# Optimization experiments

Measured on AMD Instinct MI355X. Metric: run time of the kernel, lower is better.

Reference implementation:

```python
import jax, jax.numpy as jnp
import numpy as np

D_MODEL = 1024
N_HEADS = 16
D_K = D_MODEL // N_HEADS
ROPE_THETA = 10000.0


def setup_inputs() -> dict:
    key = jax.random.key(0)
    ks = jax.random.split(key, 5)
    B, S = 2, 2048
    std = (2.0 / (D_MODEL + D_MODEL)) ** 0.5
    x = jax.random.normal(ks[0], (B, S, D_MODEL), dtype=jnp.float32)
    Wq = jax.random.normal(ks[1], (D_MODEL, D_MODEL), dtype=jnp.float32) * std
    Wk = jax.random.normal(ks[2], (D_MODEL, D_MODEL), dtype=jnp.float32) * std
    Wv = jax.random.normal(ks[3], (D_MODEL, D_MODEL), dtype=jnp.float32) * std
    Wo = jax.random.normal(ks[4], (D_MODEL, D_MODEL), dtype=jnp.float32) * std
    token_positions = jnp.arange(S, dtype=jnp.int64 if jax.config.jax_enable_x64 else jnp.int32)
    return {"x": x, "Wq": Wq, "Wk": Wk, "Wv": Wv, "Wo": Wo,
            "token_positions": token_positions}


def _apply_rope(t, token_positions):
    # t: [B, H, S, d_k]; token_positions: [S]
    inv_freq = 1.0 / (ROPE_THETA ** (jnp.arange(0, D_K, 2, dtype=jnp.float32) / D_K))  # [d_k/2]
    freqs = token_positions.astype(jnp.float32)[:, None] * inv_freq[None, :]  # [S, d_k/2]
    cos, sin = jnp.cos(freqs), jnp.sin(freqs)
    x1, x2 = t[..., ::2], t[..., 1::2]
    xr = x1 * cos - x2 * sin
    yr = x1 * sin + x2 * cos
    # interleave back to even/odd positions
    out = jnp.stack([xr, yr], axis=-1).reshape(t.shape)
    return out


def reference(x, Wq, Wk, Wv, Wo, token_positions):
    B, S, D = x.shape
    H, dk = N_HEADS, D_K
    # projections: weight is [d_out, d_in], applied as x @ W.T
    def proj_heads(W):
        y = jnp.einsum('bsd,ed->bse', x, W)
        return y.reshape(B, S, H, dk).transpose(0, 2, 1, 3)  # [B,H,S,dk]
    q = proj_heads(Wq)
    k = proj_heads(Wk)
    v = proj_heads(Wv)
    q = _apply_rope(q, token_positions)
    k = _apply_rope(k, token_positions)
    scores = jnp.einsum('bhqd,bhkd->bhqk', q, k) / jnp.sqrt(jnp.float32(dk))
    causal = jnp.tril(jnp.ones((S, S), dtype=bool))
    scores = jnp.where(causal, scores, -jnp.inf)
    attn = jax.nn.softmax(scores, axis=-1)
    out = jnp.einsum('bhqk,bhkd->bhqd', attn, v)  # [B,H,S,dk]
    out = out.transpose(0, 2, 1, 3).reshape(B, S, D)
    return jnp.einsum('bsd,ed->bse', out, Wo)
```

## Files before the change

### kernel.cpp

```cpp
#include <hip/hip_runtime.h>

typedef __bf16 bf16x8 __attribute__((ext_vector_type(8)));
typedef float f32x4 __attribute__((ext_vector_type(4)));
typedef unsigned short u16x8 __attribute__((ext_vector_type(8)));


__device__ __forceinline__ unsigned short f2bf(float f) {
  unsigned u = __builtin_bit_cast(unsigned, f);
  u = (u + 0x7FFFu + ((u >> 16) & 1u)) >> 16;
  return (unsigned short)u;
}

__device__ __forceinline__ void load_lds16(const void* g, void* l) {
  __builtin_amdgcn_global_load_lds(
      (__attribute__((address_space(1))) void*)g,
      (__attribute__((address_space(3))) void*)l, 16, 0, 0);
}

__global__ __launch_bounds__(256) void k_convert(
    const float* __restrict__ x,
    const float* __restrict__ wq, const float* __restrict__ wk,
    const float* __restrict__ wv, const float* __restrict__ wo,
    unsigned short* __restrict__ xb,
    unsigned short* __restrict__ wqb, unsigned short* __restrict__ wkb,
    unsigned short* __restrict__ wvb, unsigned short* __restrict__ wob) {
  const int g = blockIdx.x * 256 + threadIdx.x;
  const float* src;
  unsigned short* dst;
  int off;
  if (g < (1 << 20)) {
    src = x; dst = xb; off = g;
  } else {
    const int q = g - (1 << 20);
    const int t = q >> 18;
    off = q & ((1 << 18) - 1);
    src = (t == 0) ? wq : (t == 1) ? wk : (t == 2) ? wv : wo;
    dst = (t == 0) ? wqb : (t == 1) ? wkb : (t == 2) ? wvb : wob;
  }
  const float4 v = ((const float4*)src)[off];
  ushort4 r;
  r.x = f2bf(v.x); r.y = f2bf(v.y); r.z = f2bf(v.z); r.w = f2bf(v.w);
  ((ushort4*)dst)[off] = r;
}

__global__ __launch_bounds__(256) void k_rope_tab(const int* __restrict__ tpos,
                                                  float* __restrict__ ct,
                                                  float* __restrict__ st) {
  const int idx = blockIdx.x * 256 + threadIdx.x;
  const int s = idx >> 5, i = idx & 31;
  const double p = (double)tpos[s];
  const double f = p * pow(10000.0, -(double)(2 * i) / 64.0);
  ct[idx] = (float)cos(f);
  st[idx] = (float)sin(f);
}

__device__ __forceinline__ void gemm_core_1024(
    const unsigned short* __restrict__ Ag,
    const unsigned short* __restrict__ Bg,
    unsigned short* As, unsigned short* Bs, f32x4 (&acc)[4][4], int tid) {
  const int lane = tid & 63;
  const int w = tid >> 6;
  const int wm = (w >> 1) * 64;
  const int wn = (w & 1) * 64;
  const int lr = lane & 15;
  const int lg8 = (lane >> 4) * 8;
  const int c0 = tid, c1 = 256 + tid;
  const int ar0 = c0 >> 2, ac0 = (c0 & 3) * 8;
  const int ar1 = c1 >> 2, ac1 = (c1 & 3) * 8;

  auto stage = [&](int buf, int kt) {
    unsigned short* Ab = As + buf * 4096;
    unsigned short* Bb = Bs + buf * 4096;
    load_lds16(Ag + ar0 * 1024 + kt + ac0, Ab + c0 * 8);
    load_lds16(Ag + ar1 * 1024 + kt + ac1, Ab + c1 * 8);
    load_lds16(Bg + ar0 * 1024 + kt + ac0, Bb + c0 * 8);
    load_lds16(Bg + ar1 * 1024 + kt + ac1, Bb + c1 * 8);
  };

  stage(0, 0);
  stage(1, 32);
  int cur = 0;
  for (int ki = 0; ki < 32; ++ki) {
    if (ki + 2 < 32) {
      int nb = cur + 2; if (nb >= 3) nb -= 3;
      stage(nb, (ki + 2) * 32);
      asm volatile("s_waitcnt vmcnt(8)" ::: "memory");
    } else if (ki + 1 < 32) {
      asm volatile("s_waitcnt vmcnt(4)" ::: "memory");
    } else {
      asm volatile("s_waitcnt vmcnt(0)" ::: "memory");
    }
    __builtin_amdgcn_s_barrier();
    const unsigned short* Ab = As + cur * 4096;
    const unsigned short* Bb = Bs + cur * 4096;
    bf16x8 af[4], bfv[4];
#pragma unroll
    for (int mi = 0; mi < 4; ++mi)
      af[mi] = *(const bf16x8*)(Ab + (wm + mi * 16 + lr) * 32 + lg8);
#pragma unroll
    for (int ni = 0; ni < 4; ++ni)
      bfv[ni] = *(const bf16x8*)(Bb + (wn + ni * 16 + lr) * 32 + lg8);
    __builtin_amdgcn_s_setprio(1);
#pragma unroll
    for (int mi = 0; mi < 4; ++mi)
#pragma unroll
      for (int ni = 0; ni < 4; ++ni)
        acc[mi][ni] = __builtin_amdgcn_mfma_f32_16x16x32_bf16(
            af[mi], bfv[ni], acc[mi][ni], 0, 0, 0);
    __builtin_amdgcn_s_setprio(0);
    __builtin_amdgcn_s_barrier();
    ++cur; if (cur == 3) cur = 0;
  }
}

__global__ __launch_bounds__(256) void k_proj(
    const unsigned short* __restrict__ Xb,
    const unsigned short* __restrict__ Wq, const unsigned short* __restrict__ Wk,
    const unsigned short* __restrict__ Wv,
    const float* __restrict__ ctab, const float* __restrict__ stab,
    unsigned short* __restrict__ Qo, unsigned short* __restrict__ Ko,
    unsigned short* __restrict__ Vo) {
  __shared__ __align__(16) unsigned short As[3 * 128 * 32];
  __shared__ __align__(16) unsigned short Bs[3 * 128 * 32];
  const int z = blockIdx.z;
  const unsigned short* Wsel = (z == 0) ? Wq : (z == 1) ? Wk : Wv;
  unsigned short* Out = (z == 0) ? Qo : (z == 1) ? Ko : Vo;
  const int tid = threadIdx.x;
  const int bm = blockIdx.x * 128, bn = blockIdx.y * 128;
  f32x4 acc[4][4] = {};
  gemm_core_1024(Xb + (size_t)bm * 1024, Wsel + (size_t)bn * 1024, As, Bs, acc, tid);

  const int lane = tid & 63, w = tid >> 6;
  const int wm = (w >> 1) * 64, wn = (w & 1) * 64;
  const int lr = lane & 15, lg = lane >> 4;
  const bool rope = (z < 2);
  const bool odd = lane & 1;
#pragma unroll
  for (int mi = 0; mi < 4; ++mi) {
#pragma unroll
    for (int ni = 0; ni < 4; ++ni) {
#pragma unroll
      for (int reg = 0; reg < 4; ++reg) {
        const int r = bm + wm + mi * 16 + lg * 4 + reg;
        const int e = bn + wn + ni * 16 + lr;
        float val = acc[mi][ni][reg];
        const float partner = __shfl_xor(val, 1);
        const int s = r & 2047, b = r >> 11;
        const int h = e >> 6, d = e & 63;
        float outv = val;
        if (rope) {
          const int i = d >> 1;
          const float c = ctab[s * 32 + i];
          const float sn = stab[s * 32 + i];
          outv = odd ? (val * c + partner * sn) : (val * c - partner * sn);
        }
        if (z == 2)
          Out[((size_t)(b * 16 + h) * 64 + d) * 2048 + s] = f2bf(outv);
        else
          Out[((size_t)(b * 16 + h) * 2048 + s) * 64 + d] = f2bf(outv);
      }
    }
  }
}

__global__ __launch_bounds__(64, 2) void k_attn(
    const unsigned short* __restrict__ Q, const unsigned short* __restrict__ K,
    const unsigned short* __restrict__ Vt, unsigned short* __restrict__ O) {
  __shared__ __align__(16) unsigned short Vs[64 * 64];
  __shared__ __align__(16) unsigned short Pl[32 * 68];
  const int L = blockIdx.x;
  const int bh = (L & 7) * 4 + ((L >> 3) & 3);
  const int p = L >> 5;
  const int qrowA = p * 16, qrowB = (127 - p) * 16;
  const int lane = threadIdx.x & 63;
  const int lr = lane & 15, lg = lane >> 4;
  const unsigned short* Qg = Q + (size_t)bh * 2048 * 64;
  const unsigned short* Kg = K + (size_t)bh * 2048 * 64;
  const unsigned short* Vg = Vt + (size_t)bh * 64 * 2048;
  const int Ta = (qrowA + 79) >> 6;
  const int Tb = (qrowB + 79) >> 6;

  bf16x8 qfA[2], qfB[2];
#pragma unroll
  for (int h = 0; h < 2; ++h) {
    qfA[h] = *(const bf16x8*)(Qg + (qrowA + lr) * 64 + h * 32 + lg * 8);
    qfB[h] = *(const bf16x8*)(Qg + (qrowB + lr) * 64 + h * 32 + lg * 8);
  }

  u16x8 ouv;
#pragma unroll
  for (int j = 0; j < 8; ++j) ouv[j] = 0x3F80;
  const bf16x8 onesf = __builtin_bit_cast(bf16x8, ouv);

  f32x4 oA[4] = {}, oB[4] = {};
  float mA[4], lA[4], mB[4], lB[4];
#pragma unroll
  for (int r = 0; r < 4; ++r) {
    mA[r] = -__builtin_inff(); lA[r] = 0.f;
    mB[r] = -__builtin_inff(); lB[r] = 0.f;
  }

  const float SCL = 0.125f * 1.44269504088896f;

  const int kbase = lr * 64 + lg * 8;
  const unsigned short* Knext = Kg;
  const int vbase = (lane >> 3) * 2048 + (((lane & 7) ^ (lane >> 3)) * 8);
  const unsigned short* Vnext = Vg;
  unsigned short* Vw = &Vs[0];

  auto loadK = [&](bf16x8 (&kd)[4][2]) {
#pragma unroll
    for (int nt = 0; nt < 4; ++nt)
#pragma unroll
      for (int h = 0; h < 2; ++h)
        kd[nt][h] = *(const bf16x8*)(Knext + nt * 1024 + h * 32 + kbase);
    Knext += 4096;
  };
  auto issueV = [&]() {
#pragma unroll
    for (int i0 = 0; i0 < 8; ++i0)
      load_lds16(Vnext + i0 * 16384 + vbase, Vw + i0 * 512 + lane * 8);
    Vnext += 64;
  };

  auto softmax = [&](f32x4 (&s)[4], float (&m)[4], float (&l)[4], f32x4 (&oa)[4],
                     int qrow, bool needmask, int kv0, int rowbase) {
    float pm[4];
#pragma unroll
    for (int r = 0; r < 4; ++r) pm[r] = -__builtin_inff();
#pragma unroll
    for (int nt = 0; nt < 4; ++nt)
#pragma unroll
      for (int reg = 0; reg < 4; ++reg) {
        float sv = s[nt][reg];
        if (needmask) {
          const int kg = kv0 + nt * 16 + lr;
          const int qg = qrow + lg * 4 + reg;
          if (kg > qg) sv = -__builtin_inff();
        }
        s[nt][reg] = sv;
        pm[reg] = fmaxf(pm[reg], sv);
      }
#pragma unroll
    for (int off = 1; off < 16; off <<= 1)
#pragma unroll
      for (int reg = 0; reg < 4; ++reg)
        pm[reg] = fmaxf(pm[reg], __shfl_xor(pm[reg], off));

    float gm = -1.f;
#pragma unroll
    for (int reg = 0; reg < 4; ++reg) gm = fmaxf(gm, pm[reg] - m[reg]);
    float msc[4];
    if (__any(gm > 0.f)) {
#pragma unroll
      for (int reg = 0; reg < 4; ++reg) {
        const float mn = fmaxf(m[reg], pm[reg]);
        const float al = exp2f(SCL * (m[reg] - mn));
        m[reg] = mn;
        msc[reg] = SCL * mn;
        l[reg] *= al;
#pragma unroll
        for (int nt = 0; nt < 4; ++nt) oa[nt][reg] *= al;
      }
    } else {
#pragma unroll
      for (int reg = 0; reg < 4; ++reg) msc[reg] = SCL * m[reg];
    }
#pragma unroll
    for (int nt = 0; nt < 4; ++nt)
#pragma unroll
      for (int reg = 0; reg < 4; ++reg) {
        const float pv = exp2f(s[nt][reg] * SCL - msc[reg]);
        Pl[(rowbase + lg * 4 + reg) * 68 + nt * 16 + lr] = f2bf(pv);
      }
  };

  bf16x8 kA_[4][2], kB_[4][2];
  loadK(kA_);
  issueV();

  auto body = [&](int t, bf16x8 (&kc)[4][2], bf16x8 (&kn)[4][2]) {
    const int kv0 = t * 64;
    const bool more = (t + 1 < Tb);
    const bool actA = (t < Ta);
    if (more) loadK(kn);

    f32x4 sB_[4];
    __builtin_amdgcn_s_setprio(1);
#pragma unroll
    for (int nt = 0; nt < 4; ++nt) {
      f32x4 z = {0.f, 0.f, 0.f, 0.f};
      z = __builtin_amdgcn_mfma_f32_16x16x32_bf16(qfB[0], kc[nt][0], z, 0, 0, 0);
      sB_[nt] = __builtin_amdgcn_mfma_f32_16x16x32_bf16(qfB[1], kc[nt][1], z, 0, 0, 0);
    }
    __builtin_amdgcn_s_setprio(0);
    softmax(sB_, mB, lB, oB, qrowB, t == Tb - 1, kv0, 16);

    if (actA) {
      f32x4 sA_[4];
      __builtin_amdgcn_s_setprio(1);
#pragma unroll
      for (int nt = 0; nt < 4; ++nt) {
        f32x4 z = {0.f, 0.f, 0.f, 0.f};
        z = __builtin_amdgcn_mfma_f32_16x16x32_bf16(qfA[0], kc[nt][0], z, 0, 0, 0);
        sA_[nt] = __builtin_amdgcn_mfma_f32_16x16x32_bf16(qfA[1], kc[nt][1], z, 0, 0, 0);
      }
      __builtin_amdgcn_s_setprio(0);
      softmax(sA_, mA, lA, oA, qrowA, t == Ta - 1, kv0, 0);
    }

    bf16x8 paA[2], paB[2];
#pragma unroll
    for (int ks = 0; ks < 2; ++ks) {
      paB[ks] = *(const bf16x8*)(Pl + (16 + lr) * 68 + ks * 32 + lg * 8);
      if (actA) paA[ks] = *(const bf16x8*)(Pl + lr * 68 + ks * 32 + lg * 8);
    }

    if (more) asm volatile("s_waitcnt vmcnt(8)" ::: "memory");
    else      asm volatile("s_waitcnt vmcnt(0)" ::: "memory");

    __builtin_amdgcn_s_setprio(1);
    {
      f32x4 z = {0.f, 0.f, 0.f, 0.f};
      z = __builtin_amdgcn_mfma_f32_16x16x32_bf16(paB[0], onesf, z, 0, 0, 0);
      z = __builtin_amdgcn_mfma_f32_16x16x32_bf16(paB[1], onesf, z, 0, 0, 0);
#pragma unroll
      for (int reg = 0; reg < 4; ++reg) lB[reg] += z[reg];
    }
    if (actA) {
      f32x4 z = {0.f, 0.f, 0.f, 0.f};
      z = __builtin_amdgcn_mfma_f32_16x16x32_bf16(paA[0], onesf, z, 0, 0, 0);
      z = __builtin_amdgcn_mfma_f32_16x16x32_bf16(paA[1], onesf, z, 0, 0, 0);
#pragma unroll
      for (int reg = 0; reg < 4; ++reg) lA[reg] += z[reg];
    }
#pragma unroll
    for (int nt = 0; nt < 4; ++nt) {
      const int row = nt * 16 + lr;
      const bf16x8 vb0 = *(const bf16x8*)(Vw + row * 64 + ((lg ^ (row & 7)) * 8));
      const bf16x8 vb1 = *(const bf16x8*)(Vw + row * 64 + (((lg + 4) ^ (row & 7)) * 8));
      oB[nt] = __builtin_amdgcn_mfma_f32_16x16x32_bf16(paB[0], vb0, oB[nt], 0, 0, 0);
      oB[nt] = __builtin_amdgcn_mfma_f32_16x16x32_bf16(paB[1], vb1, oB[nt], 0, 0, 0);
      if (actA) {
        oA[nt] = __builtin_amdgcn_mfma_f32_16x16x32_bf16(paA[0], vb0, oA[nt], 0, 0, 0);
        oA[nt] = __builtin_amdgcn_mfma_f32_16x16x32_bf16(paA[1], vb1, oA[nt], 0, 0, 0);
      }
    }
    __builtin_amdgcn_s_setprio(0);

    asm volatile("s_waitcnt lgkmcnt(0)" ::: "memory");
    if (more) issueV();
  };

  int t = 0;
  for (;;) {
    body(t, kA_, kB_); ++t; if (t >= Tb) break;
    body(t, kB_, kA_); ++t; if (t >= Tb) break;
  }

  const int b = bh >> 4, h = bh & 15;
#pragma unroll
  for (int reg = 0; reg < 4; ++reg) {
    const float invA = 1.0f / lA[reg];
    const float invB = 1.0f / lB[reg];
    const int sA_ = qrowA + lg * 4 + reg;
    const int sB_ = qrowB + lg * 4 + reg;
#pragma unroll
    for (int nt = 0; nt < 4; ++nt) {
      const int dv = nt * 16 + lr;
      O[((size_t)b * 2048 + sA_) * 1024 + h * 64 + dv] = f2bf(oA[nt][reg] * invA);
      O[((size_t)b * 2048 + sB_) * 1024 + h * 64 + dv] = f2bf(oB[nt][reg] * invB);
    }
  }
}

__global__ __launch_bounds__(256) void k_out(const unsigned short* __restrict__ Ab,
                                             const unsigned short* __restrict__ Wo,
                                             float* __restrict__ Out) {
  __shared__ __align__(16) unsigned short As[3 * 128 * 32];
  __shared__ __align__(16) unsigned short Bs[3 * 128 * 32];
  const int tid = threadIdx.x;
  const int bm = blockIdx.x * 128, bn = blockIdx.y * 128;
  f32x4 acc[4][4] = {};
  gemm_core_1024(Ab + (size_t)bm * 1024, Wo + (size_t)bn * 1024, As, Bs, acc, tid);
  const int lane = tid & 63, w = tid >> 6;
  const int wm = (w >> 1) * 64, wn = (w & 1) * 64;
  const int lr = lane & 15, lg = lane >> 4;
#pragma unroll
  for (int mi = 0; mi < 4; ++mi)
#pragma unroll
    for (int ni = 0; ni < 4; ++ni)
#pragma unroll
      for (int reg = 0; reg < 4; ++reg) {
        const int r = bm + wm + mi * 16 + lg * 4 + reg;
        const int e = bn + wn + ni * 16 + lr;
        Out[(size_t)r * 1024 + e] = acc[mi][ni][reg];
      }
}

extern "C" void kernel_launch(void* const* d_in, const int* in_sizes, int n_in,
                              void* d_out, int out_size, void* d_ws, size_t ws_size,
                              hipStream_t stream) {
  const float* x = (const float*)d_in[0];
  const float* Wq = (const float*)d_in[1];
  const float* Wk = (const float*)d_in[2];
  const float* Wv = (const float*)d_in[3];
  const float* Wo = (const float*)d_in[4];
  const int* tpos = (const int*)d_in[5];
  float* out = (float*)d_out;
  char* ws = (char*)d_ws;
  const size_t MB = 1024 * 1024;
  unsigned short* xb = (unsigned short*)(ws);
  unsigned short* wqb = (unsigned short*)(ws + 8 * MB);
  unsigned short* wkb = (unsigned short*)(ws + 10 * MB);
  unsigned short* wvb = (unsigned short*)(ws + 12 * MB);
  unsigned short* wob = (unsigned short*)(ws + 14 * MB);
  unsigned short* Qb = (unsigned short*)(ws + 16 * MB);
  unsigned short* Kb = (unsigned short*)(ws + 24 * MB);
  unsigned short* Vtb = (unsigned short*)(ws + 32 * MB);
  unsigned short* Ab = (unsigned short*)(ws + 40 * MB);
  float* ctab = (float*)(ws + 48 * MB);
  float* stab = (float*)(ws + 48 * MB + 256 * 1024);

  k_convert<<<dim3(8192), dim3(256), 0, stream>>>(x, Wq, Wk, Wv, Wo, xb, wqb, wkb,
                                                  wvb, wob);
  k_rope_tab<<<dim3(256), dim3(256), 0, stream>>>(tpos, ctab, stab);
  k_proj<<<dim3(32, 8, 3), dim3(256), 0, stream>>>(xb, wqb, wkb, wvb, ctab, stab,
                                                   Qb, Kb, Vtb);
  k_attn<<<dim3(2048), dim3(64), 0, stream>>>(Qb, Kb, Vtb, Ab);
  k_out<<<dim3(32, 8), dim3(256), 0, stream>>>(Ab, wob, out);
}
```

Measured before the change: 158.6 us.

## Split paired causal q-tiles into independent single-tile attention blocks

Each attention block previously processed two 16-row query tiles (p and 127-p) so every block did the same amount of causal work. Now each block handles one 16-row tile, the grid is doubled to 4096, and launch bounds allow 4 waves per SIMD. The K register double-buffering is dropped, so K loads are issued inside each iteration and waited on before use. P is converted with the packed v_cvt_pk_bf16_f32 instruction. Per-block work becomes uneven (early tiles are tiny), so load balance now depends on the scheduler, and the exposed K load latency may hurt unless the added occupancy hides it.

```diff
diff --git a/kernel.cpp b/kernel.cpp
--- a/kernel.cpp
+++ b/kernel.cpp
@@ -9,6 +9,12 @@
   unsigned u = __builtin_bit_cast(unsigned, f);
   u = (u + 0x7FFFu + ((u >> 16) & 1u)) >> 16;
   return (unsigned short)u;
+}
+
+__device__ __forceinline__ unsigned cvt_pk_bf16(float lo, float hi) {
+  unsigned r;
+  asm("v_cvt_pk_bf16_f32 %0, %1, %2" : "=v"(r) : "v"(lo), "v"(hi));
+  return r;
 }
 
 __device__ __forceinline__ void load_lds16(const void* g, void* l) {
@@ -163,42 +169,36 @@
   }
 }
 
-__global__ __launch_bounds__(64, 2) void k_attn(
+__global__ __launch_bounds__(64, 4) void k_attn(
     const unsigned short* __restrict__ Q, const unsigned short* __restrict__ K,
     const unsigned short* __restrict__ Vt, unsigned short* __restrict__ O) {
   __shared__ __align__(16) unsigned short Vs[64 * 64];
-  __shared__ __align__(16) unsigned short Pl[32 * 68];
+  __shared__ __align__(16) unsigned short Pl[16 * 68];
   const int L = blockIdx.x;
   const int bh = (L & 7) * 4 + ((L >> 3) & 3);
   const int p = L >> 5;
-  const int qrowA = p * 16, qrowB = (127 - p) * 16;
+  const int qrow = p * 16;
+  const int T = (qrow + 79) >> 6;
   const int lane = threadIdx.x & 63;
   const int lr = lane & 15, lg = lane >> 4;
   const unsigned short* Qg = Q + (size_t)bh * 2048 * 64;
   const unsigned short* Kg = K + (size_t)bh * 2048 * 64;
   const unsigned short* Vg = Vt + (size_t)bh * 64 * 2048;
-  const int Ta = (qrowA + 79) >> 6;
-  const int Tb = (qrowB + 79) >> 6;
-
-  bf16x8 qfA[2], qfB[2];
-#pragma unroll
-  for (int h = 0; h < 2; ++h) {
-    qfA[h] = *(const bf16x8*)(Qg + (qrowA + lr) * 64 + h * 32 + lg * 8);
-    qfB[h] = *(const bf16x8*)(Qg + (qrowB + lr) * 64 + h * 32 + lg * 8);
-  }
+
+  bf16x8 qf[2];
+#pragma unroll
+  for (int h = 0; h < 2; ++h)
+    qf[h] = *(const bf16x8*)(Qg + (qrow + lr) * 64 + h * 32 + lg * 8);
 
   u16x8 ouv;
 #pragma unroll
   for (int j = 0; j < 8; ++j) ouv[j] = 0x3F80;
   const bf16x8 onesf = __builtin_bit_cast(bf16x8, ouv);
 
-  f32x4 oA[4] = {}, oB[4] = {};
-  float mA[4], lA[4], mB[4], lB[4];
-#pragma unroll
-  for (int r = 0; r < 4; ++r) {
-    mA[r] = -__builtin_inff(); lA[r] = 0.f;
-    mB[r] = -__builtin_inff(); lB[r] = 0.f;
-  }
+  f32x4 oacc[4] = {};
+  float m[4], l[4];
+#pragma unroll
+  for (int r = 0; r < 4; ++r) { m[r] = -__builtin_inff(); l[r] = 0.f; }
 
   const float SCL = 0.125f * 1.44269504088896f;
 
@@ -208,14 +208,6 @@
   const unsigned short* Vnext = Vg;
   unsigned short* Vw = &Vs[0];
 
-  auto loadK = [&](bf16x8 (&kd)[4][2]) {
-#pragma unroll
-    for (int nt = 0; nt < 4; ++nt)
-#pragma unroll
-      for (int h = 0; h < 2; ++h)
-        kd[nt][h] = *(const bf16x8*)(Knext + nt * 1024 + h * 32 + kbase);
-    Knext += 4096;
-  };
   auto issueV = [&]() {
 #pragma unroll
     for (int i0 = 0; i0 < 8; ++i0)
@@ -223,8 +215,28 @@
     Vnext += 64;
   };
 
-  auto softmax = [&](f32x4 (&s)[4], float (&m)[4], float (&l)[4], f32x4 (&oa)[4],
-                     int qrow, bool needmask, int kv0, int rowbase) {
+  issueV();
+
+  for (int t = 0; t < T; ++t) {
+    bf16x8 kd[4][2];
+#pragma unroll
+    for (int nt = 0; nt < 4; ++nt)
+#pragma unroll
+      for (int h = 0; h < 2; ++h)
+        kd[nt][h] = *(const bf16x8*)(Knext + nt * 1024 + h * 32 + kbase);
+    Knext += 4096;
+
+    f32x4 sacc[4];
+    __builtin_amdgcn_s_setprio(1);
+#pragma unroll
+    for (int nt = 0; nt < 4; ++nt) {
+      f32x4 z = {0.f, 0.f, 0.f, 0.f};
+      z = __builtin_amdgcn_mfma_f32_16x16x32_bf16(qf[0], kd[nt][0], z, 0, 0, 0);
+      sacc[nt] = __builtin_amdgcn_mfma_f32_16x16x32_bf16(qf[1], kd[nt][1], z, 0, 0, 0);
+    }
+    __builtin_amdgcn_s_setprio(0);
+
+    const bool needmask = (t == T - 1);
     float pm[4];
 #pragma unroll
     for (int r = 0; r < 4; ++r) pm[r] = -__builtin_inff();
@@ -232,13 +244,13 @@
     for (int nt = 0; nt < 4; ++nt)
 #pragma unroll
       for (int reg = 0; reg < 4; ++reg) {
-        float sv = s[nt][reg];
+        float sv = sacc[nt][reg];
         if (needmask) {
-          const int kg = kv0 + nt * 16 + lr;
+          const int kg = t * 64 + nt * 16 + lr;
           const int qg = qrow + lg * 4 + reg;
           if (kg > qg) sv = -__builtin_inff();
         }
-        s[nt][reg] = sv;
+        sacc[nt][reg] = sv;
         pm[reg] = fmaxf(pm[reg], sv);
       }
 #pragma unroll
@@ -260,116 +272,65 @@
         msc[reg] = SCL * mn;
         l[reg] *= al;
 #pragma unroll
-        for (int nt = 0; nt < 4; ++nt) oa[nt][reg] *= al;
+        for (int nt = 0; nt < 4; ++nt) oacc[nt][reg] *= al;
       }
     } else {
 #pragma unroll
       for (int reg = 0; reg < 4; ++reg) msc[reg] = SCL * m[reg];
     }
-#pragma unroll
-    for (int nt = 0; nt < 4; ++nt)
-#pragma unroll
-      for (int reg = 0; reg < 4; ++reg) {
-        const float pv = exp2f(s[nt][reg] * SCL - msc[reg]);
-        Pl[(rowbase + lg * 4 + reg) * 68 + nt * 16 + lr] = f2bf(pv);
-      }
-  };
-
-  bf16x8 kA_[4][2], kB_[4][2];
-  loadK(kA_);
-  issueV();
-
-  auto body = [&](int t, bf16x8 (&kc)[4][2], bf16x8 (&kn)[4][2]) {
-    const int kv0 = t * 64;
-    const bool more = (t + 1 < Tb);
-    const bool actA = (t < Ta);
-    if (more) loadK(kn);
-
-    f32x4 sB_[4];
-    __builtin_amdgcn_s_setprio(1);
+
 #pragma unroll
     for (int nt = 0; nt < 4; ++nt) {
-      f32x4 z = {0.f, 0.f, 0.f, 0.f};
-      z = __builtin_amdgcn_mfma_f32_16x16x32_bf16(qfB[0], kc[nt][0], z, 0, 0, 0);
-      sB_[nt] = __builtin_amdgcn_mfma_f32_16x16x32_bf16(qfB[1], kc[nt][1], z, 0, 0, 0);
-    }
-    __builtin_amdgcn_s_setprio(0);
-    softmax(sB_, mB, lB, oB, qrowB, t == Tb - 1, kv0, 16);
-
-    if (actA) {
-      f32x4 sA_[4];
-      __builtin_amdgcn_s_setprio(1);
-#pragma unroll
-      for (int nt = 0; nt < 4; ++nt) {
-        f32x4 z = {0.f, 0.f, 0.f, 0.f};
-        z = __builtin_amdgcn_mfma_f32_16x16x32_bf16(qfA[0], kc[nt][0], z, 0, 0, 0);
-        sA_[nt] = __builtin_amdgcn_mfma_f32_16x16x32_bf16(qfA[1], kc[nt][1], z, 0, 0, 0);
-      }
-      __builtin_amdgcn_s_setprio(0);
-      softmax(sA_, mA, lA, oA, qrowA, t == Ta - 1, kv0, 0);
-    }
-
-    bf16x8 paA[2], paB[2];
-#pragma unroll
-    for (int ks = 0; ks < 2; ++ks) {
-      paB[ks] = *(const bf16x8*)(Pl + (16 + lr) * 68 + ks * 32 + lg * 8);
-      if (actA) paA[ks] = *(const bf16x8*)(Pl + lr * 68 + ks * 32 + lg * 8);
-    }
-
-    if (more) asm volatile("s_waitcnt vmcnt(8)" ::: "memory");
-    else      asm volatile("s_waitcnt vmcnt(0)" ::: "memory");
+      const float p0 = exp2f(sacc[nt][0] * SCL - msc[0]);
+      const float p1 = exp2f(sacc[nt][1] * SCL - msc[1]);
+      const float p2 = exp2f(sacc[nt][2] * SCL - msc[2]);
+      const float p3 = exp2f(sacc[nt][3] * SCL - msc[3]);
+      const unsigned w01 = cvt_pk_bf16(p0, p1);
+      const unsigned w23 = cvt_pk_bf16(p2, p3);
+      unsigned short* base = Pl + (lg * 4) * 68 + nt * 16 + lr;
+      base[0] = (unsigned short)w01;
+      base[68] = (unsigned short)(w01 >> 16);
+      base[136] = (unsigned short)w23;
+      base[204] = (unsigned short)(w23 >> 16);
+    }
+    bf16x8 pa[2];
+#pragma unroll
+    for (int ks = 0; ks < 2; ++ks)
+      pa[ks] = *(const bf16x8*)(Pl + lr * 68 + ks * 32 + lg * 8);
+
+    asm volatile("s_waitcnt vmcnt(0)" ::: "memory");
 
     __builtin_amdgcn_s_setprio(1);
     {
       f32x4 z = {0.f, 0.f, 0.f, 0.f};
-      z = __builtin_amdgcn_mfma_f32_16x16x32_bf16(paB[0], onesf, z, 0, 0, 0);
-      z = __builtin_amdgcn_mfma_f32_16x16x32_bf16(paB[1], onesf, z, 0, 0, 0);
-#pragma unroll
-      for (int reg = 0; reg < 4; ++reg) lB[reg] += z[reg];
-    }
-    if (actA) {
-      f32x4 z = {0.f, 0.f, 0.f, 0.f};
-      z = __builtin_amdgcn_mfma_f32_16x16x32_bf16(paA[0], onesf, z, 0, 0, 0);
-      z = __builtin_amdgcn_mfma_f32_16x16x32_bf16(paA[1], onesf, z, 0, 0, 0);
-#pragma unroll
-      for (int reg = 0; reg < 4; ++reg) lA[reg] += z[reg];
+      z = __builtin_amdgcn_mfma_f32_16x16x32_bf16(pa[0], onesf, z, 0, 0, 0);
+      z = __builtin_amdgcn_mfma_f32_16x16x32_bf16(pa[1], onesf, z, 0, 0, 0);
+#pragma unroll
+      for (int reg = 0; reg < 4; ++reg) l[reg] += z[reg];
     }
 #pragma unroll
     for (int nt = 0; nt < 4; ++nt) {
       const int row = nt * 16 + lr;
       const bf16x8 vb0 = *(const bf16x8*)(Vw + row * 64 + ((lg ^ (row & 7)) * 8));
       const bf16x8 vb1 = *(const bf16x8*)(Vw + row * 64 + (((lg + 4) ^ (row & 7)) * 8));
-      oB[nt] = __builtin_amdgcn_mfma_f32_16x16x32_bf16(paB[0], vb0, oB[nt], 0, 0, 0);
-      oB[nt] = __builtin_amdgcn_mfma_f32_16x16x32_bf16(paB[1], vb1, oB[nt], 0, 0, 0);
-      if (actA) {
-        oA[nt] = __builtin_amdgcn_mfma_f32_16x16x32_bf16(paA[0], vb0, oA[nt], 0, 0, 0);
-        oA[nt] = __builtin_amdgcn_mfma_f32_16x16x32_bf16(paA[1], vb1, oA[nt], 0, 0, 0);
-      }
+      oacc[nt] = __builtin_amdgcn_mfma_f32_16x16x32_bf16(pa[0], vb0, oacc[nt], 0, 0, 0);
+      oacc[nt] = __builtin_amdgcn_mfma_f32_16x16x32_bf16(pa[1], vb1, oacc[nt], 0, 0, 0);
     }
     __builtin_amdgcn_s_setprio(0);
 
     asm volatile("s_waitcnt lgkmcnt(0)" ::: "memory");
-    if (more) issueV();
-  };
-
-  int t = 0;
-  for (;;) {
-    body(t, kA_, kB_); ++t; if (t >= Tb) break;
-    body(t, kB_, kA_); ++t; if (t >= Tb) break;
+    if (t + 1 < T) issueV();
   }
 
   const int b = bh >> 4, h = bh & 15;
 #pragma unroll
   for (int reg = 0; reg < 4; ++reg) {
-    const float invA = 1.0f / lA[reg];
-    const float invB = 1.0f / lB[reg];
-    const int sA_ = qrowA + lg * 4 + reg;
-    const int sB_ = qrowB + lg * 4 + reg;
+    const float inv = 1.0f / l[reg];
+    const int s = qrow + lg * 4 + reg;
 #pragma unroll
     for (int nt = 0; nt < 4; ++nt) {
       const int dv = nt * 16 + lr;
-      O[((size_t)b * 2048 + sA_) * 1024 + h * 64 + dv] = f2bf(oA[nt][reg] * invA);
-      O[((size_t)b * 2048 + sB_) * 1024 + h * 64 + dv] = f2bf(oB[nt][reg] * invB);
+      O[((size_t)b * 2048 + s) * 1024 + h * 64 + dv] = f2bf(oacc[nt][reg] * inv);
     }
   }
 }
@@ -427,6 +388,6 @@
   k_rope_tab<<<dim3(256), dim3(256), 0, stream>>>(tpos, ctab, stab);
   k_proj<<<dim3(32, 8, 3), dim3(256), 0, stream>>>(xb, wqb, wkb, wvb, ctab, stab,
                                                    Qb, Kb, Vtb);
-  k_attn<<<dim3(2048), dim3(64), 0, stream>>>(Qb, Kb, Vtb, Ab);
+  k_attn<<<dim3(4096), dim3(64), 0, stream>>>(Qb, Kb, Vtb, Ab);
   k_out<<<dim3(32, 8), dim3(256), 0, stream>>>(Ab, wob, out);
 }
```

Measured after the change: 179.8 us. +13.3%, slower.
